# Optimization experiments

Hardware: AMD Instinct MI355X
Metric: run time of the kernel (lower is better)

Reference implementation:

```python
import jax, jax.numpy as jnp
import numpy as np

L, B, S, D, H, DK, F = 6, 4, 2048, 512, 8, 64, 2048


def setup_inputs() -> dict:
    key = jax.random.key(0)
    ks = iter(jax.random.split(key, 40))
    def rn(shape, scale=0.02):
        return jax.random.normal(next(ks), shape, jnp.float32) * scale
    inp = {
        "x": jax.random.normal(next(ks), (B, S, D), jnp.float32),
        "enc": jax.random.normal(next(ks), (B, S, D), jnp.float32),
    }
    for pre in ("sa", "ca"):
        inp[f"{pre}_wq"] = rn((L, D, H * DK)); inp[f"{pre}_bq"] = jnp.zeros((L, H * DK), jnp.float32)
        inp[f"{pre}_wk"] = rn((L, D, H * DK)); inp[f"{pre}_bk"] = jnp.zeros((L, H * DK), jnp.float32)
        inp[f"{pre}_wv"] = rn((L, D, H * DK)); inp[f"{pre}_bv"] = jnp.zeros((L, H * DK), jnp.float32)
        inp[f"{pre}_wo"] = rn((L, H * DK, D)); inp[f"{pre}_bo"] = jnp.zeros((L, D), jnp.float32)
    for i in (1, 2, 3):
        inp[f"ln{i}_g"] = jnp.ones((L, D), jnp.float32)
        inp[f"ln{i}_b"] = jnp.zeros((L, D), jnp.float32)
    inp["ff_w1"] = rn((L, D, F)); inp["ff_b1"] = jnp.zeros((L, F), jnp.float32)
    inp["ff_w2"] = rn((L, F, D)); inp["ff_b2"] = jnp.zeros((L, D), jnp.float32)
    return inp


def _layer_norm(z, g, b, eps=1e-5):
    m = z.mean(-1, keepdims=True)
    v = z.var(-1, keepdims=True)
    return (z - m) * jax.lax.rsqrt(v + eps) * g + b


def _mha(q_in, kv_in, wq, bq, wk, bk, wv, bv, wo, bo, causal_bias):
    b, s, _ = q_in.shape
    Q = (q_in @ wq + bq).reshape(b, s, H, DK)   # [B,S,H,DK]
    K = (kv_in @ wk + bk).reshape(b, s, H, DK)
    V = (kv_in @ wv + bv).reshape(b, s, H, DK)
    scores = jnp.einsum("bqhd,bkhd->bhqk", Q, K) / jnp.float32(DK) ** 0.5
    if causal_bias is not None:
        scores = scores + causal_bias  # additive -inf above diagonal
    w = jax.nn.softmax(scores, axis=-1)
    att = jnp.einsum("bhqk,bkhd->bqhd", w, V).reshape(b, s, H * DK)
    return att @ wo + bo


def reference(x, enc, sa_wq, sa_bq, sa_wk, sa_bk, sa_wv, sa_bv, sa_wo, sa_bo,
              ca_wq, ca_bq, ca_wk, ca_bk, ca_wv, ca_bv, ca_wo, ca_bo,
              ln1_g, ln1_b, ln2_g, ln2_b, ln3_g, ln3_b,
              ff_w1, ff_b1, ff_w2, ff_b2):
    s = x.shape[1]
    causal_bias = jnp.triu(jnp.full((s, s), -jnp.inf, jnp.float32), 1)

    params = (sa_wq, sa_bq, sa_wk, sa_bk, sa_wv, sa_bv, sa_wo, sa_bo,
              ca_wq, ca_bq, ca_wk, ca_bk, ca_wv, ca_bv, ca_wo, ca_bo,
              ln1_g, ln1_b, ln2_g, ln2_b, ln3_g, ln3_b,
              ff_w1, ff_b1, ff_w2, ff_b2)

    def block(h, p):
        (swq, sbq, swk, sbk, swv, sbv, swo, sbo,
         cwq, cbq, cwk, cbk, cwv, cbv, cwo, cbo,
         g1, b1, g2, b2, g3, b3, w1, bb1, w2, bb2) = p
        # masked self-attention + residual + LN  (faithful to source)
        x1 = _layer_norm(h + _mha(h, h, swq, sbq, swk, sbk, swv, sbv, swo, sbo, causal_bias), g1, b1)
        # cross-attention; residual comes from the BLOCK INPUT h (source bug kept)
        y = _layer_norm(h + _mha(x1, enc, cwq, cbq, cwk, cbk, cwv, cbv, cwo, cbo, None), g2, b2)
        # FFN; residual from x1 (source bug kept)
        out = _layer_norm(x1 + (jax.nn.relu(y @ w1 + bb1) @ w2 + bb2), g3, b3)
        return out, None

    out, _ = jax.lax.scan(block, x, params)
    return out
```

## Files before the change

kernel.cpp:

```cpp
#include <hip/hip_runtime.h>
#include <stdint.h>

#define LCOUNT 6
#define BB 4
#define SS 2048
#define DD 512
#define HH 8
#define DKK 64
#define FFDIM 2048
#define MM (BB*SS)

typedef __attribute__((ext_vector_type(8))) __bf16 bf16x8;
typedef __attribute__((ext_vector_type(4))) float f32x4;
typedef unsigned short u16;

__device__ __forceinline__ u16 f2bf(float f) {
  union { __bf16 h; u16 u; } v; v.h = (__bf16)f; return v.u;
}
__device__ __forceinline__ float bf2f(u16 u) {
  union { uint32_t u; float f; } v; v.u = ((uint32_t)u) << 16;
  return v.f;
}

__device__ __forceinline__ void gload_lds16(const u16* gsrc, u16* ldst) {
  __builtin_amdgcn_global_load_lds((const __attribute__((address_space(1))) char*)gsrc,
                                   (__attribute__((address_space(3))) char*)ldst, 16, 0, 0);
}

__global__ __launch_bounds__(256) void f2bf_kernel(const float* __restrict__ in,
                                                   u16* __restrict__ outp, int n) {
  int i = (blockIdx.x * 256 + threadIdx.x) * 8;
  if (i >= n) return;
  float4 a = *(const float4*)&in[i];
  float4 b = *(const float4*)&in[i + 4];
  union { u16 us[8]; uint4 v; } pk;
  pk.us[0] = f2bf(a.x); pk.us[1] = f2bf(a.y); pk.us[2] = f2bf(a.z); pk.us[3] = f2bf(a.w);
  pk.us[4] = f2bf(b.x); pk.us[5] = f2bf(b.y); pk.us[6] = f2bf(b.z); pk.us[7] = f2bf(b.w);
  *(uint4*)&outp[i] = pk.v;
}

__global__ __launch_bounds__(256) void bias_cat(const float* a, const float* b, const float* c,
                                                float* dst, int n, int total) {
  int i = blockIdx.x * 256 + threadIdx.x;
  if (i >= total) return;
  int parts = (c != nullptr) ? 3 : 2;
  int per = parts * n;
  int l = i / per, cc = i % per;
  const float* s = cc < n ? a : (cc < 2 * n ? b : c);
  dst[i] = s[l * n + (cc % n)];
}

__global__ __launch_bounds__(256) void wtrans(const float* __restrict__ W,
                                              u16* __restrict__ Wt, int K_, int N_,
                                              size_t lstride) {
  __shared__ float tile[64 * 65];
  const int l = blockIdx.z;
  const float* Wl = W + (size_t)l * K_ * N_;
  u16* Wtl = Wt + (size_t)l * lstride;
  const int n0 = blockIdx.x * 64, k0 = blockIdx.y * 64;
  const int tid = threadIdx.x;
  const int r = tid >> 2, c4 = (tid & 3) * 16;
#pragma unroll
  for (int j = 0; j < 16; j += 4) {
    float4 v = *(const float4*)&Wl[(size_t)(k0 + r) * N_ + n0 + c4 + j];
    tile[r * 65 + c4 + j + 0] = v.x;
    tile[r * 65 + c4 + j + 1] = v.y;
    tile[r * 65 + c4 + j + 2] = v.z;
    tile[r * 65 + c4 + j + 3] = v.w;
  }
  __syncthreads();
  const int nr = tid >> 2, kc = (tid & 3) * 16;
#pragma unroll
  for (int half = 0; half < 2; ++half) {
    union { u16 us[8]; uint4 v; } pk;
#pragma unroll
    for (int e = 0; e < 8; ++e) pk.us[e] = f2bf(tile[(kc + half * 8 + e) * 65 + nr]);
    *(uint4*)&Wtl[(size_t)(n0 + nr) * K_ + k0 + kc + half * 8] = pk.v;
  }
}

template <int BMT, int BKT, bool RELU, bool VT>
__global__ __launch_bounds__(256)
void gemm_bt(const u16* __restrict__ A, const u16* __restrict__ Bt,
             const float* __restrict__ bias, u16* __restrict__ C,
             int N_, int K_, int CS, u16* __restrict__ vt, int vtc0) {
  constexpr int MR = BMT / 32;
  constexpr int CH = BKT / 8;
  constexpr int RPR = 2048 / BKT;
  constexpr int KS = BKT / 32;
  __shared__ u16 As[BMT * BKT];
  __shared__ u16 Bs[128 * BKT];
  const int tid = threadIdx.x;
  const int wid = tid >> 6, lane = tid & 63;
  const int l15 = lane & 15, g = lane >> 4;
  const int wr = wid >> 1, wc = wid & 1;
  const int lrow = (CH == 8) ? (lane >> 3) : (lane >> 4);
  const int lch  = lane & (CH - 1);
  const int wrows = 64 / CH;
  const int lin = blockIdx.x + gridDim.x * blockIdx.y;
  const int nwg = gridDim.x * gridDim.y;
  const int swz = (lin & 7) * (nwg >> 3) + (lin >> 3);
  const int brow = (swz / gridDim.x) * BMT;
  const int bcol = (swz % gridDim.x) * 128;

  f32x4 acc[MR][4];
#pragma unroll
  for (int m = 0; m < MR; ++m)
#pragma unroll
    for (int n = 0; n < 4; ++n) acc[m][n] = (f32x4){0.f, 0.f, 0.f, 0.f};

  for (int kt = 0; kt < K_; kt += BKT) {
#pragma unroll
    for (int r = 0; r < BMT / RPR; ++r) {
      int row = r * RPR + wid * wrows + lrow;
      int slot = lch ^ (row & 7);
      gload_lds16(A + (size_t)(brow + row) * K_ + kt + slot * 8,
                  &As[r * 2048 + wid * 512]);
    }
#pragma unroll
    for (int r = 0; r < 128 / RPR; ++r) {
      int row = r * RPR + wid * wrows + lrow;
      int slot = lch ^ (row & 7);
      gload_lds16(Bt + (size_t)(bcol + row) * K_ + kt + slot * 8,
                  &Bs[r * 2048 + wid * 512]);
    }
    __syncthreads();
#pragma unroll
    for (int ks = 0; ks < KS; ++ks) {
      bf16x8 af[MR], bfr[4];
#pragma unroll
      for (int m = 0; m < MR; ++m) {
        int row = wr * (BMT / 2) + m * 16 + l15;
        int slot = (ks * 4 + g) ^ (row & 7);
        af[m] = *(const bf16x8*)&As[row * BKT + slot * 8];
      }
#pragma unroll
      for (int n = 0; n < 4; ++n) {
        int row = wc * 64 + n * 16 + l15;
        int slot = (ks * 4 + g) ^ (row & 7);
        bfr[n] = *(const bf16x8*)&Bs[row * BKT + slot * 8];
      }
#pragma unroll
      for (int m = 0; m < MR; ++m)
#pragma unroll
        for (int n = 0; n < 4; ++n)
          acc[m][n] = __builtin_amdgcn_mfma_f32_16x16x32_bf16(af[m], bfr[n], acc[m][n], 0, 0, 0);
    }
    __syncthreads();
  }
#pragma unroll
  for (int n = 0; n < 4; ++n) {
    int col = bcol + wc * 64 + n * 16 + l15;
    float bv = bias ? bias[col] : 0.f;
    if (VT && col >= vtc0) {
      int hh = (col - vtc0) >> 6, dd = (col - vtc0) & 63;
#pragma unroll
      for (int m = 0; m < MR; ++m) {
        int s0g = brow + wr * (BMT / 2) + m * 16 + g * 4;
        int bb = s0g >> 11, ss = s0g & (SS - 1);
        union { u16 us[4]; uint2 v; } pk;
#pragma unroll
        for (int r = 0; r < 4; ++r) pk.us[r] = f2bf(acc[m][n][r] + bv);
        *(uint2*)&vt[(((size_t)(bb * HH + hh)) * DKK + dd) * SS + ss] = pk.v;
      }
    } else {
#pragma unroll
      for (int m = 0; m < MR; ++m) {
#pragma unroll
        for (int r = 0; r < 4; ++r) {
          int rowg = brow + wr * (BMT / 2) + m * 16 + g * 4 + r;
          float v = acc[m][n][r] + bv;
          if (RELU) v = fmaxf(v, 0.f);
          C[(size_t)rowg * CS + col] = f2bf(v);
        }
      }
    }
  }
}

template <bool CAUSAL>
__global__ __launch_bounds__(256, 4)
void attn_kernel(const u16* __restrict__ Qm, const u16* __restrict__ Km,
                 const u16* __restrict__ Vt, u16* __restrict__ Om, int qks) {
  __shared__ u16 Ks[2][64 * 64];
  __shared__ u16 Vs[2][64 * 64];
  __shared__ u16 Ps[4][16 * 64];
  const int lin = blockIdx.x;
  const int bh = (lin & 7) * 4 + ((lin >> 3) >> 5);
  const int qc = (lin >> 3) & 31;
  const int qb = (qc & 1) ? (31 - (qc >> 1)) : (qc >> 1);
  const int h = bh & 7, b = bh >> 3;
  const int tid = threadIdx.x, wid = tid >> 6, lane = tid & 63;
  const int l15 = lane & 15, g = lane >> 4;
  const int qstart = qb * 64;
  const size_t qbase = ((size_t)b * SS) * qks + h * DKK;
  const size_t vtbase = (size_t)(b * HH + h) * DKK * SS;
  const size_t obase = ((size_t)b * SS) * DD + h * DKK;
  u16* psw = &Ps[wid][0];
  const int srow = wid * 8 + (lane >> 3);
  const int sslot = lane & 7;
  const int qg = qstart + wid * 16 + l15;
  const int pswz = (l15 & 7) << 1;
  const float SC = 0.18033688f;

  const u16* kp = Km + qbase;
  const u16* vp = Vt + vtbase;

  bf16x8 qf[2];
#pragma unroll
  for (int ks = 0; ks < 2; ++ks)
    qf[ks] = *(const bf16x8*)&Qm[qbase + (size_t)qg * qks + ks * 32 + g * 8];

  f32x4 oacc[4];
#pragma unroll
  for (int nb = 0; nb < 4; ++nb) oacc[nb] = (f32x4){0.f, 0.f, 0.f, 0.f};
  float m_run = -3.0e38f, l_run = 0.f;

  const int T = CAUSAL ? (qb + 1) : (SS / 64);

#pragma unroll
  for (int r = 0; r < 2; ++r) {
    int row = r * 32 + srow;
    int slot = sslot ^ (row & 7);
    gload_lds16(kp + (size_t)row * qks + slot * 8, &Ks[0][r * 2048 + wid * 512]);
    gload_lds16(vp + (size_t)row * SS + slot * 8, &Vs[0][r * 2048 + wid * 512]);
  }
  __syncthreads();

  int cur = 0;
  for (int t = 0; t < T; ++t) {
    const int kstart = t * 64;
    if (t + 1 < T) {
#pragma unroll
      for (int r = 0; r < 2; ++r) {
        int row = r * 32 + srow;
        int slot = sslot ^ (row & 7);
        gload_lds16(kp + (size_t)(kstart + 64 + row) * qks + slot * 8,
                    &Ks[cur ^ 1][r * 2048 + wid * 512]);
        gload_lds16(vp + (size_t)row * SS + kstart + 64 + slot * 8,
                    &Vs[cur ^ 1][r * 2048 + wid * 512]);
      }
    }
    f32x4 sacc[4];
#pragma unroll
    for (int nb = 0; nb < 4; ++nb) sacc[nb] = (f32x4){0.f, 0.f, 0.f, 0.f};
    __builtin_amdgcn_s_setprio(1);
#pragma unroll
    for (int nb = 0; nb < 4; ++nb) {
      int row = nb * 16 + l15;
#pragma unroll
      for (int ks = 0; ks < 2; ++ks) {
        bf16x8 kf = *(const bf16x8*)&Ks[cur][row * 64 + (((ks * 4 + g) ^ (row & 7)) * 8)];
        sacc[nb] = __builtin_amdgcn_mfma_f32_16x16x32_bf16(kf, qf[ks], sacc[nb], 0, 0, 0);
      }
    }
    __builtin_amdgcn_s_setprio(0);
    if (CAUSAL && t == T - 1) {
#pragma unroll
      for (int nb = 0; nb < 4; ++nb)
#pragma unroll
        for (int r = 0; r < 4; ++r)
          if ((kstart + nb * 16 + g * 4 + r) > qg) sacc[nb][r] = -3.0e38f;
    }
    f32x4 m4 = sacc[0];
#pragma unroll
    for (int nb = 1; nb < 4; ++nb) {
      m4[0] = fmaxf(m4[0], sacc[nb][0]); m4[1] = fmaxf(m4[1], sacc[nb][1]);
      m4[2] = fmaxf(m4[2], sacc[nb][2]); m4[3] = fmaxf(m4[3], sacc[nb][3]);
    }
    float mx = fmaxf(fmaxf(m4[0], m4[1]), fmaxf(m4[2], m4[3]));
    mx = fmaxf(mx, __shfl_xor(mx, 16));
    mx = fmaxf(mx, __shfl_xor(mx, 32));
    const bool skip = __all(mx <= m_run + 64.0f);
    float mnew = skip ? m_run : fmaxf(m_run, mx);
    float mc = mnew * SC;
    float s = 0.f;
#pragma unroll
    for (int nb = 0; nb < 4; ++nb) {
#pragma unroll
      for (int r = 0; r < 4; ++r) {
        float e = __builtin_amdgcn_exp2f(sacc[nb][r] * SC - mc);
        sacc[nb][r] = e; s += e;
      }
    }
    s += __shfl_xor(s, 16);
    s += __shfl_xor(s, 32);
    if (skip) {
      l_run += s;
    } else {
      float resc = __builtin_amdgcn_exp2f((m_run - mnew) * SC);
      l_run = l_run * resc + s;
      m_run = mnew;
      float ro[4];
#pragma unroll
      for (int r = 0; r < 4; ++r) ro[r] = __shfl(resc, g * 4 + r);
#pragma unroll
      for (int nb = 0; nb < 4; ++nb)
#pragma unroll
        for (int r = 0; r < 4; ++r) oacc[nb][r] *= ro[r];
    }
#pragma unroll
    for (int nb = 0; nb < 4; ++nb) {
      union { u16 us[4]; uint2 v; } pk;
#pragma unroll
      for (int r = 0; r < 4; ++r) pk.us[r] = f2bf(sacc[nb][r]);
      int cp = (nb * 4 + g) ^ pswz;
      *(uint2*)&psw[l15 * 64 + cp * 4] = pk.v;
    }
    bf16x8 pf[2];
#pragma unroll
    for (int ks = 0; ks < 2; ++ks) {
      int cp0 = (8 * ks + 2 * g) ^ pswz;
      pf[ks] = *(const bf16x8*)&psw[l15 * 64 + cp0 * 4];
    }
    __builtin_amdgcn_s_setprio(1);
#pragma unroll
    for (int nb = 0; nb < 4; ++nb) {
      int row = nb * 16 + l15;
#pragma unroll
      for (int ks = 0; ks < 2; ++ks) {
        bf16x8 vf = *(const bf16x8*)&Vs[cur][row * 64 + (((ks * 4 + g) ^ (row & 7)) * 8)];
        oacc[nb] = __builtin_amdgcn_mfma_f32_16x16x32_bf16(pf[ks], vf, oacc[nb], 0, 0, 0);
      }
    }
    __builtin_amdgcn_s_setprio(0);
    __syncthreads();
    cur ^= 1;
  }
  float linv = 1.f / l_run;
  float io[4];
#pragma unroll
  for (int r = 0; r < 4; ++r) io[r] = __shfl(linv, g * 4 + r);
#pragma unroll
  for (int nb = 0; nb < 4; ++nb) {
#pragma unroll
    for (int r = 0; r < 4; ++r) {
      Om[obase + (size_t)(qstart + wid * 16 + g * 4 + r) * DD + nb * 16 + l15] =
          f2bf(oacc[nb][r] * io[r]);
    }
  }
}

__global__ __launch_bounds__(256)
void ln_kernel(const u16* __restrict__ A, const u16* __restrict__ Bv,
               const float* __restrict__ gamma, const float* __restrict__ beta,
               u16* __restrict__ out_bf, float* __restrict__ out_f32) {
  const int row = blockIdx.x * 4 + (threadIdx.x >> 6);
  const int lane = threadIdx.x & 63;
  uint4 av = *(const uint4*)&A[(size_t)row * DD + lane * 8];
  uint4 bv = *(const uint4*)&Bv[(size_t)row * DD + lane * 8];
  const u16* au = (const u16*)&av;
  const u16* bu = (const u16*)&bv;
  float z[8], s = 0.f, s2 = 0.f;
#pragma unroll
  for (int j = 0; j < 8; ++j) {
    float x = bf2f(au[j]) + bf2f(bu[j]);
    z[j] = x; s += x; s2 += x * x;
  }
#pragma unroll
  for (int off = 1; off < 64; off <<= 1) {
    s += __shfl_xor(s, off);
    s2 += __shfl_xor(s2, off);
  }
  float mean = s * (1.f / 512.f);
  float var = s2 * (1.f / 512.f) - mean * mean;
  float rs = rsqrtf(var + 1e-5f);
  union { u16 us[8]; uint4 v; } pk;
#pragma unroll
  for (int j = 0; j < 8; ++j) {
    float o = (z[j] - mean) * rs * gamma[lane * 8 + j] + beta[lane * 8 + j];
    pk.us[j] = f2bf(o);
    if (out_f32) out_f32[(size_t)row * DD + lane * 8 + j] = o;
  }
  *(uint4*)&out_bf[(size_t)row * DD + lane * 8] = pk.v;
}

extern "C" void kernel_launch(void* const* d_in, const int* in_sizes, int n_in,
                              void* d_out, int out_size, void* d_ws, size_t ws_size,
                              hipStream_t stream) {
  const float* x   = (const float*)d_in[0];
  const float* enc = (const float*)d_in[1];
  const float* sa_w[4] = {(const float*)d_in[2], (const float*)d_in[4], (const float*)d_in[6], (const float*)d_in[8]};
  const float* sa_b[4] = {(const float*)d_in[3], (const float*)d_in[5], (const float*)d_in[7], (const float*)d_in[9]};
  const float* ca_w[4] = {(const float*)d_in[10], (const float*)d_in[12], (const float*)d_in[14], (const float*)d_in[16]};
  const float* ca_b[4] = {(const float*)d_in[11], (const float*)d_in[13], (const float*)d_in[15], (const float*)d_in[17]};
  const float* ln_g[3] = {(const float*)d_in[18], (const float*)d_in[20], (const float*)d_in[22]};
  const float* ln_b[3] = {(const float*)d_in[19], (const float*)d_in[21], (const float*)d_in[23]};
  const float* ffw1 = (const float*)d_in[24];
  const float* ffb1 = (const float*)d_in[25];
  const float* ffw2 = (const float*)d_in[26];
  const float* ffb2 = (const float*)d_in[27];

  char* ws = (char*)d_ws;
  size_t o = 0;
  auto take = [&](size_t bytes) {
    void* p = ws + o;
    o += (bytes + 255) & ~(size_t)255;
    return p;
  };
  u16* wqkv  = (u16*)take((size_t)LCOUNT * 1536 * 512 * 2);
  u16* wqca  = (u16*)take((size_t)LCOUNT * 512 * 512 * 2);
  u16* wkvca = (u16*)take((size_t)LCOUNT * 1024 * 512 * 2);
  u16* wosa  = (u16*)take((size_t)LCOUNT * 512 * 512 * 2);
  u16* woca  = (u16*)take((size_t)LCOUNT * 512 * 512 * 2);
  u16* w1t   = (u16*)take((size_t)LCOUNT * 512 * 2048 * 2);
  u16* w2t   = (u16*)take((size_t)LCOUNT * 2048 * 512 * 2);
  float* bqkv = (float*)take((size_t)LCOUNT * 1536 * 4);
  float* bkv  = (float*)take((size_t)LCOUNT * 1024 * 4);
  u16* Hb   = (u16*)take((size_t)MM * 512 * 2);
  u16* Eb   = (u16*)take((size_t)MM * 512 * 2);
  u16* QKVb = (u16*)take((size_t)MM * 1536 * 2);
  u16* Ab   = (u16*)take((size_t)MM * 512 * 2);
  u16* Pb   = (u16*)take((size_t)MM * 512 * 2);
  u16* X1b  = (u16*)take((size_t)MM * 512 * 2);
  u16* Yb   = (u16*)take((size_t)MM * 512 * 2);
  u16* Fb   = (u16*)take((size_t)MM * 2048 * 2);
  u16* Vtb  = Fb;

  f2bf_kernel<<<2048, 256, 0, stream>>>(x, Hb, MM * 512);
  f2bf_kernel<<<2048, 256, 0, stream>>>(enc, Eb, MM * 512);
  wtrans<<<dim3(8, 8, LCOUNT), 256, 0, stream>>>(sa_w[0], wqkv,              512, 512, (size_t)1536 * 512);
  wtrans<<<dim3(8, 8, LCOUNT), 256, 0, stream>>>(sa_w[1], wqkv + 512 * 512,  512, 512, (size_t)1536 * 512);
  wtrans<<<dim3(8, 8, LCOUNT), 256, 0, stream>>>(sa_w[2], wqkv + 1024 * 512, 512, 512, (size_t)1536 * 512);
  wtrans<<<dim3(8, 8, LCOUNT), 256, 0, stream>>>(sa_w[3], wosa,              512, 512, (size_t)512 * 512);
  wtrans<<<dim3(8, 8, LCOUNT), 256, 0, stream>>>(ca_w[0], wqca,              512, 512, (size_t)512 * 512);
  wtrans<<<dim3(8, 8, LCOUNT), 256, 0, stream>>>(ca_w[1], wkvca,             512, 512, (size_t)1024 * 512);
  wtrans<<<dim3(8, 8, LCOUNT), 256, 0, stream>>>(ca_w[2], wkvca + 512 * 512, 512, 512, (size_t)1024 * 512);
  wtrans<<<dim3(8, 8, LCOUNT), 256, 0, stream>>>(ca_w[3], woca,              512, 512, (size_t)512 * 512);
  wtrans<<<dim3(32, 8, LCOUNT), 256, 0, stream>>>(ffw1, w1t, 512, 2048, (size_t)2048 * 512);
  wtrans<<<dim3(8, 32, LCOUNT), 256, 0, stream>>>(ffw2, w2t, 2048, 512, (size_t)512 * 2048);
  bias_cat<<<36, 256, 0, stream>>>(sa_b[0], sa_b[1], sa_b[2], bqkv, 512, LCOUNT * 1536);
  bias_cat<<<24, 256, 0, stream>>>(ca_b[1], ca_b[2], nullptr, bkv, 512, LCOUNT * 1024);

  for (int l = 0; l < LCOUNT; ++l) {
    const size_t w512 = (size_t)l * 512 * 512;
    const size_t wff = (size_t)l * 512 * 2048;
    gemm_bt<128, 64, false, true><<<dim3(12, 64), 256, 0, stream>>>(
        Hb, wqkv + (size_t)l * 1536 * 512, bqkv + l * 1536, QKVb, 1536, 512, 1536, Vtb, 1024);
    attn_kernel<true><<<dim3(1024), 256, 0, stream>>>(QKVb, QKVb + 512, Vtb, Ab, 1536);
    gemm_bt<64, 128, false, false><<<dim3(4, 128), 256, 0, stream>>>(
        Ab, wosa + w512, sa_b[3] + l * 512, Pb, 512, 512, 512, nullptr, 0);
    ln_kernel<<<MM / 4, 256, 0, stream>>>(Hb, Pb, ln_g[0] + l * 512, ln_b[0] + l * 512, X1b, nullptr);
    gemm_bt<64, 128, false, false><<<dim3(4, 128), 256, 0, stream>>>(
        X1b, wqca + w512, ca_b[0] + l * 512, QKVb, 512, 512, 1536, nullptr, 0);
    gemm_bt<128, 64, false, true><<<dim3(8, 64), 256, 0, stream>>>(
        Eb, wkvca + (size_t)l * 1024 * 512, bkv + l * 1024, QKVb + 512, 1024, 512, 1536, Vtb, 512);
    attn_kernel<false><<<dim3(1024), 256, 0, stream>>>(QKVb, QKVb + 512, Vtb, Ab, 1536);
    gemm_bt<64, 128, false, false><<<dim3(4, 128), 256, 0, stream>>>(
        Ab, woca + w512, ca_b[3] + l * 512, Pb, 512, 512, 512, nullptr, 0);
    ln_kernel<<<MM / 4, 256, 0, stream>>>(Hb, Pb, ln_g[1] + l * 512, ln_b[1] + l * 512, Yb, nullptr);
    gemm_bt<128, 64, true, false><<<dim3(16, 64), 256, 0, stream>>>(
        Yb, w1t + wff, ffb1 + l * 2048, Fb, 2048, 512, 2048, nullptr, 0);
    gemm_bt<64, 128, false, false><<<dim3(4, 128), 256, 0, stream>>>(
        Fb, w2t + wff, ffb2 + l * 512, Pb, 512, 2048, 512, nullptr, 0);
    ln_kernel<<<MM / 4, 256, 0, stream>>>(X1b, Pb, ln_g[2] + l * 512, ln_b[2] + l * 512, Hb,
                                          (l == LCOUNT - 1) ? (float*)d_out : nullptr);
  }
}
```

Baseline: 1.854 ms.

## Use 64x64 tiles for N=512 GEMMs and shuffle P fragments via registers

The GEMM template gains a BN tile parameter. The four N=512 projections now use 64x64 output tiles with twice as many workgroups, which raises occupancy and parallelism on the 256 CUs at the cost of less operand reuse per tile. In the attention kernel, the per-wave LDS staging of the softmax probabilities is replaced by cross-lane shuffles that rebuild the MFMA A-operand layout in registers. This removes the LDS write/read round trip and frees LDS, but adds shuffle instructions.

```diff
diff --git a/kernel.cpp b/kernel.cpp
--- a/kernel.cpp
+++ b/kernel.cpp
@@ -13,6 +13,7 @@
 typedef __attribute__((ext_vector_type(8))) __bf16 bf16x8;
 typedef __attribute__((ext_vector_type(4))) float f32x4;
 typedef unsigned short u16;
+typedef unsigned long long u64;
 
 __device__ __forceinline__ u16 f2bf(float f) {
   union { __bf16 h; u16 u; } v; v.h = (__bf16)f; return v.u;
@@ -79,17 +80,18 @@
   }
 }
 
-template <int BMT, int BKT, bool RELU, bool VT>
+template <int BMT, int BNT, int BKT, bool RELU, bool VT>
 __global__ __launch_bounds__(256)
 void gemm_bt(const u16* __restrict__ A, const u16* __restrict__ Bt,
              const float* __restrict__ bias, u16* __restrict__ C,
              int N_, int K_, int CS, u16* __restrict__ vt, int vtc0) {
   constexpr int MR = BMT / 32;
+  constexpr int NR = BNT / 32;
   constexpr int CH = BKT / 8;
   constexpr int RPR = 2048 / BKT;
   constexpr int KS = BKT / 32;
   __shared__ u16 As[BMT * BKT];
-  __shared__ u16 Bs[128 * BKT];
+  __shared__ u16 Bs[BNT * BKT];
   const int tid = threadIdx.x;
   const int wid = tid >> 6, lane = tid & 63;
   const int l15 = lane & 15, g = lane >> 4;
@@ -101,13 +103,13 @@
   const int nwg = gridDim.x * gridDim.y;
   const int swz = (lin & 7) * (nwg >> 3) + (lin >> 3);
   const int brow = (swz / gridDim.x) * BMT;
-  const int bcol = (swz % gridDim.x) * 128;
-
-  f32x4 acc[MR][4];
+  const int bcol = (swz % gridDim.x) * BNT;
+
+  f32x4 acc[MR][NR];
 #pragma unroll
   for (int m = 0; m < MR; ++m)
 #pragma unroll
-    for (int n = 0; n < 4; ++n) acc[m][n] = (f32x4){0.f, 0.f, 0.f, 0.f};
+    for (int n = 0; n < NR; ++n) acc[m][n] = (f32x4){0.f, 0.f, 0.f, 0.f};
 
   for (int kt = 0; kt < K_; kt += BKT) {
 #pragma unroll
@@ -118,7 +120,7 @@
                   &As[r * 2048 + wid * 512]);
     }
 #pragma unroll
-    for (int r = 0; r < 128 / RPR; ++r) {
+    for (int r = 0; r < BNT / RPR; ++r) {
       int row = r * RPR + wid * wrows + lrow;
       int slot = lch ^ (row & 7);
       gload_lds16(Bt + (size_t)(bcol + row) * K_ + kt + slot * 8,
@@ -127,7 +129,7 @@
     __syncthreads();
 #pragma unroll
     for (int ks = 0; ks < KS; ++ks) {
-      bf16x8 af[MR], bfr[4];
+      bf16x8 af[MR], bfr[NR];
 #pragma unroll
       for (int m = 0; m < MR; ++m) {
         int row = wr * (BMT / 2) + m * 16 + l15;
@@ -135,22 +137,22 @@
         af[m] = *(const bf16x8*)&As[row * BKT + slot * 8];
       }
 #pragma unroll
-      for (int n = 0; n < 4; ++n) {
-        int row = wc * 64 + n * 16 + l15;
+      for (int n = 0; n < NR; ++n) {
+        int row = wc * (BNT / 2) + n * 16 + l15;
         int slot = (ks * 4 + g) ^ (row & 7);
         bfr[n] = *(const bf16x8*)&Bs[row * BKT + slot * 8];
       }
 #pragma unroll
       for (int m = 0; m < MR; ++m)
 #pragma unroll
-        for (int n = 0; n < 4; ++n)
+        for (int n = 0; n < NR; ++n)
           acc[m][n] = __builtin_amdgcn_mfma_f32_16x16x32_bf16(af[m], bfr[n], acc[m][n], 0, 0, 0);
     }
     __syncthreads();
   }
 #pragma unroll
-  for (int n = 0; n < 4; ++n) {
-    int col = bcol + wc * 64 + n * 16 + l15;
+  for (int n = 0; n < NR; ++n) {
+    int col = bcol + wc * (BNT / 2) + n * 16 + l15;
     float bv = bias ? bias[col] : 0.f;
     if (VT && col >= vtc0) {
       int hh = (col - vtc0) >> 6, dd = (col - vtc0) & 63;
@@ -184,7 +186,6 @@
                  const u16* __restrict__ Vt, u16* __restrict__ Om, int qks) {
   __shared__ u16 Ks[2][64 * 64];
   __shared__ u16 Vs[2][64 * 64];
-  __shared__ u16 Ps[4][16 * 64];
   const int lin = blockIdx.x;
   const int bh = (lin & 7) * 4 + ((lin >> 3) >> 5);
   const int qc = (lin >> 3) & 31;
@@ -196,12 +197,12 @@
   const size_t qbase = ((size_t)b * SS) * qks + h * DKK;
   const size_t vtbase = (size_t)(b * HH + h) * DKK * SS;
   const size_t obase = ((size_t)b * SS) * DD + h * DKK;
-  u16* psw = &Ps[wid][0];
   const int srow = wid * 8 + (lane >> 3);
   const int sslot = lane & 7;
   const int qg = qstart + wid * 16 + l15;
-  const int pswz = (l15 & 7) << 1;
   const float SC = 0.18033688f;
+  const int sA = ((2 * g) & 3) * 16 + l15;
+  const int sB = ((2 * g + 1) & 3) * 16 + l15;
 
   const u16* kp = Km + qbase;
   const u16* vp = Vt + vtbase;
@@ -299,19 +300,25 @@
 #pragma unroll
         for (int r = 0; r < 4; ++r) oacc[nb][r] *= ro[r];
     }
+    u64 pk[4];
 #pragma unroll
     for (int nb = 0; nb < 4; ++nb) {
-      union { u16 us[4]; uint2 v; } pk;
-#pragma unroll
-      for (int r = 0; r < 4; ++r) pk.us[r] = f2bf(sacc[nb][r]);
-      int cp = (nb * 4 + g) ^ pswz;
-      *(uint2*)&psw[l15 * 64 + cp * 4] = pk.v;
+      union { u16 us[4]; u64 v; } z;
+#pragma unroll
+      for (int r = 0; r < 4; ++r) z.us[r] = f2bf(sacc[nb][r]);
+      pk[nb] = z.v;
     }
     bf16x8 pf[2];
 #pragma unroll
     for (int ks = 0; ks < 2; ++ks) {
-      int cp0 = (8 * ks + 2 * g) ^ pswz;
-      pf[ks] = *(const bf16x8*)&psw[l15 * 64 + cp0 * 4];
+      u64 a0 = __shfl(pk[2 * ks], sA);
+      u64 a1 = __shfl(pk[2 * ks + 1], sA);
+      u64 b0 = __shfl(pk[2 * ks], sB);
+      u64 b1 = __shfl(pk[2 * ks + 1], sB);
+      union { u64 q[2]; bf16x8 v; } mrg;
+      mrg.q[0] = (g < 2) ? a0 : a1;
+      mrg.q[1] = (g < 2) ? b0 : b1;
+      pf[ks] = mrg.v;
     }
     __builtin_amdgcn_s_setprio(1);
 #pragma unroll
@@ -435,23 +442,23 @@
   for (int l = 0; l < LCOUNT; ++l) {
     const size_t w512 = (size_t)l * 512 * 512;
     const size_t wff = (size_t)l * 512 * 2048;
-    gemm_bt<128, 64, false, true><<<dim3(12, 64), 256, 0, stream>>>(
+    gemm_bt<128, 128, 64, false, true><<<dim3(12, 64), 256, 0, stream>>>(
         Hb, wqkv + (size_t)l * 1536 * 512, bqkv + l * 1536, QKVb, 1536, 512, 1536, Vtb, 1024);
     attn_kernel<true><<<dim3(1024), 256, 0, stream>>>(QKVb, QKVb + 512, Vtb, Ab, 1536);
-    gemm_bt<64, 128, false, false><<<dim3(4, 128), 256, 0, stream>>>(
+    gemm_bt<64, 64, 128, false, false><<<dim3(8, 128), 256, 0, stream>>>(
         Ab, wosa + w512, sa_b[3] + l * 512, Pb, 512, 512, 512, nullptr, 0);
     ln_kernel<<<MM / 4, 256, 0, stream>>>(Hb, Pb, ln_g[0] + l * 512, ln_b[0] + l * 512, X1b, nullptr);
-    gemm_bt<64, 128, false, false><<<dim3(4, 128), 256, 0, stream>>>(
+    gemm_bt<64, 64, 128, false, false><<<dim3(8, 128), 256, 0, stream>>>(
         X1b, wqca + w512, ca_b[0] + l * 512, QKVb, 512, 512, 1536, nullptr, 0);
-    gemm_bt<128, 64, false, true><<<dim3(8, 64), 256, 0, stream>>>(
+    gemm_bt<128, 128, 64, false, true><<<dim3(8, 64), 256, 0, stream>>>(
         Eb, wkvca + (size_t)l * 1024 * 512, bkv + l * 1024, QKVb + 512, 1024, 512, 1536, Vtb, 512);
     attn_kernel<false><<<dim3(1024), 256, 0, stream>>>(QKVb, QKVb + 512, Vtb, Ab, 1536);
-    gemm_bt<64, 128, false, false><<<dim3(4, 128), 256, 0, stream>>>(
+    gemm_bt<64, 64, 128, false, false><<<dim3(8, 128), 256, 0, stream>>>(
         Ab, woca + w512, ca_b[3] + l * 512, Pb, 512, 512, 512, nullptr, 0);
     ln_kernel<<<MM / 4, 256, 0, stream>>>(Hb, Pb, ln_g[1] + l * 512, ln_b[1] + l * 512, Yb, nullptr);
-    gemm_bt<128, 64, true, false><<<dim3(16, 64), 256, 0, stream>>>(
+    gemm_bt<128, 128, 64, true, false><<<dim3(16, 64), 256, 0, stream>>>(
         Yb, w1t + wff, ffb1 + l * 2048, Fb, 2048, 512, 2048, nullptr, 0);
-    gemm_bt<64, 128, false, false><<<dim3(4, 128), 256, 0, stream>>>(
+    gemm_bt<64, 64, 128, false, false><<<dim3(8, 128), 256, 0, stream>>>(
         Fb, w2t + wff, ffb2 + l * 512, Pb, 512, 2048, 512, nullptr, 0);
     ln_kernel<<<MM / 4, 256, 0, stream>>>(X1b, Pb, ln_g[2] + l * 512, ln_b[2] + l * 512, Hb,
                                           (l == LCOUNT - 1) ? (float*)d_out : nullptr);
```

Result: slower. 2.040 ms (+10.0%).
